# Kernel optimization log

Hardware: AMD Instinct MI355X
Metric: run time of the kernel (lower is better)

## Reference

```python
import jax, jax.numpy as jnp
import numpy as np

B, C, H, W, S = 32, 256, 80, 80, 2
MID = max(C // 4, 16)  # 64

def setup_inputs() -> dict:
    key = jax.random.key(0)
    k1, k2, k3, k4 = jax.random.split(key, 4)
    x = jax.random.normal(k1, (B, C, H, W), jnp.float32)
    w1 = jax.random.normal(k2, (MID, C), jnp.float32) * 0.05   # 1x1 conv, no bias
    w2 = jax.random.normal(k3, (2 * S * S, MID), jnp.float32) * 0.05
    b2 = jax.random.normal(k4, (2 * S * S,), jnp.float32) * 0.05
    return {"x": x, "w1": w1, "w2": w2, "b2": b2}

def _bilinear_border(im, gx, gy):
    # im: (C,H,W); gx,gy: (H,W) normalized coords in [-1,1]
    # matches F.grid_sample(mode='bilinear', padding_mode='border', align_corners=True)
    Hh, Ww = im.shape[1], im.shape[2]
    ix = jnp.clip((gx + 1.0) * 0.5 * (Ww - 1), 0.0, Ww - 1)  # border clamp
    iy = jnp.clip((gy + 1.0) * 0.5 * (Hh - 1), 0.0, Hh - 1)
    x0 = jnp.floor(ix); y0 = jnp.floor(iy)
    x0i = x0.astype(jnp.int32); y0i = y0.astype(jnp.int32)
    x1i = jnp.clip(x0i + 1, 0, Ww - 1); y1i = jnp.clip(y0i + 1, 0, Hh - 1)
    wx = ix - x0; wy = iy - y0
    v00 = im[:, y0i, x0i]; v01 = im[:, y0i, x1i]
    v10 = im[:, y1i, x0i]; v11 = im[:, y1i, x1i]
    return (v00 * (1 - wx) * (1 - wy) + v01 * wx * (1 - wy)
            + v10 * (1 - wx) * wy + v11 * wx * wy)

def _dysample(x, w1, w2, b2):
    Bb, Cc, Hh, Ww = x.shape
    s = S; ss = s * s
    # offset branch: 1x1 conv -> ReLU -> 1x1 conv -> tanh
    hid = jax.nn.relu(jnp.einsum('bchw,mc->bmhw', x, w1))
    off = jnp.tanh(jnp.einsum('bmhw,om->bohw', hid, w2) + b2[None, :, None, None])
    off_x, off_y = off[:, :ss], off[:, ss:]  # each (B,ss,H,W)
    H2, W2 = Hh * s, Ww * s
    ys = jnp.linspace(-1 + 1 / H2, 1 - 1 / H2, H2, dtype=x.dtype)
    xs = jnp.linspace(-1 + 1 / W2, 1 - 1 / W2, W2, dtype=x.dtype)
    gy, gx = jnp.meshgrid(ys, xs, indexing='ij')  # (H2,W2)
    def rearr(g):  # (H2,W2) -> (ss,H,W), matching the torch view/permute chain
        return g.reshape(Hh, s, Ww, s).transpose(0, 2, 1, 3).reshape(Hh, Ww, ss).transpose(2, 0, 1)
    gxb = rearr(gx)[None]; gyb = rearr(gy)[None]  # (1,ss,H,W)
    sf = 2.0 / max(H2, W2)
    sx = gxb + off_x * sf  # (B,ss,H,W)
    sy = gyb + off_y * sf
    # sample: each of the ss grids samples from the same image (no x replication)
    samp = jax.vmap(
        lambda im, gxs, gys: jax.vmap(lambda a, b: _bilinear_border(im, a, b))(gxs, gys)
    )(x, sx, sy)  # (B,ss,C,H,W)
    # pixel-shuffle rearrangement to (B,C,H*s,W*s)
    out = samp.transpose(0, 2, 1, 3, 4).reshape(Bb, Cc, s, s, Hh, Ww)
    out = out.transpose(0, 1, 4, 2, 5, 3).reshape(Bb, Cc, H2, W2)
    return out

def reference(x, w1, w2, b2):
    return _dysample(x, w1, w2, b2)
```

## Files before the change

### kernel.cpp

```cpp
#include <hip/hip_runtime.h>
#include <math.h>

#define B_   32
#define C_   256
#define H_   80
#define W_   80
#define MID_ 64
#define HW_  (H_*W_)
#define H2_  160
#define W2_  160
#define HW2_ (H2_*W2_)
#define CSPLIT_ 8
#define CCHUNK_ (C_/CSPLIT_)

__global__ __launch_bounds__(256) void transpose_w1_kernel(
    const float* __restrict__ w1, float* __restrict__ w1t)
{
    int idx = blockIdx.x * 256 + threadIdx.x;
    int m = idx & (MID_-1);
    int c = idx >> 6;
    w1t[idx] = w1[m*C_ + c];
}

__global__ __launch_bounds__(256) void offsets_kernel(
    const float* __restrict__ x, const float* __restrict__ w1t,
    const float* __restrict__ w2, const float* __restrict__ b2,
    float* __restrict__ off)
{
    int p  = blockIdx.x * 256 + threadIdx.x;
    int b  = p / HW_;
    int hw = p - b*HW_;
    const float* xp = x + (size_t)b*C_*HW_ + hw;

    float hid[MID_];
    #pragma unroll
    for (int m = 0; m < MID_; ++m) hid[m] = 0.f;

    for (int c = 0; c < C_; ++c) {
        float xv = xp[(size_t)c*HW_];
        const float* wr = w1t + c*MID_;
        #pragma unroll
        for (int m = 0; m < MID_; ++m) hid[m] = fmaf(xv, wr[m], hid[m]);
    }
    #pragma unroll
    for (int m = 0; m < MID_; ++m) hid[m] = fmaxf(hid[m], 0.f);

    float* op = off + (size_t)b*8*HW_ + hw;
    #pragma unroll
    for (int o = 0; o < 8; ++o) {
        float acc = b2[o];
        #pragma unroll
        for (int m = 0; m < MID_; ++m) acc = fmaf(hid[m], w2[o*MID_+m], acc);
        op[o*HW_] = tanhf(acc);
    }
}

__global__ __launch_bounds__(256) void sample_kernel(
    const float* __restrict__ x, const float* __restrict__ off,
    float* __restrict__ out)
{
    int p  = blockIdx.x * 256 + threadIdx.x;
    int b  = p / HW_;
    int hw = p - b*HW_;
    int h  = hw / W_;
    int w  = hw - h*W_;
    int c0 = blockIdx.y * CCHUNK_;

    const float* offp = off + (size_t)b*8*HW_ + hw;

    float wgt[4][4];
    int   ofs[4][4];
    #pragma unroll
    for (int k = 0; k < 4; ++k) {
        int i = k >> 1, j = k & 1;
        float ox = offp[k*HW_];
        float oy = offp[(4+k)*HW_];
        float gx = -1.f + (2.f*(float)(2*w+j) + 1.f) * (1.f/(float)W2_);
        float gy = -1.f + (2.f*(float)(2*h+i) + 1.f) * (1.f/(float)H2_);
        float sx = gx + ox * (2.f/(float)W2_);
        float sy = gy + oy * (2.f/(float)H2_);
        float ix = (sx + 1.f) * 0.5f * (float)(W_-1);
        float iy = (sy + 1.f) * 0.5f * (float)(H_-1);
        ix = fminf(fmaxf(ix, 0.f), (float)(W_-1));
        iy = fminf(fmaxf(iy, 0.f), (float)(H_-1));
        float xf = floorf(ix), yf = floorf(iy);
        int   x0 = (int)xf,    y0 = (int)yf;
        float wx = ix - xf,    wy = iy - yf;
        int   x1 = min(x0+1, W_-1), y1 = min(y0+1, H_-1);
        wgt[k][0] = (1.f-wx)*(1.f-wy);
        wgt[k][1] = wx*(1.f-wy);
        wgt[k][2] = (1.f-wx)*wy;
        wgt[k][3] = wx*wy;
        ofs[k][0] = y0*W_ + x0;
        ofs[k][1] = y0*W_ + x1;
        ofs[k][2] = y1*W_ + x0;
        ofs[k][3] = y1*W_ + x1;
    }

    const float* xq = x   + ((size_t)b*C_ + c0)*HW_;
    float*       oq = out + ((size_t)b*C_ + c0)*HW2_;
    int obase = (2*h)*W2_ + 2*w;

    #pragma unroll 2
    for (int ci = 0; ci < CCHUNK_; ++ci) {
        int xcb = ci*HW_;
        float v[4];
        #pragma unroll
        for (int k = 0; k < 4; ++k) {
            v[k] = xq[xcb + ofs[k][0]]*wgt[k][0] + xq[xcb + ofs[k][1]]*wgt[k][1]
                 + xq[xcb + ofs[k][2]]*wgt[k][2] + xq[xcb + ofs[k][3]]*wgt[k][3];
        }
        int ob = ci*HW2_ + obase;
        *reinterpret_cast<float2*>(oq + ob)        = make_float2(v[0], v[1]);
        *reinterpret_cast<float2*>(oq + ob + W2_)  = make_float2(v[2], v[3]);
    }
}

extern "C" void kernel_launch(void* const* d_in, const int* in_sizes, int n_in,
                              void* d_out, int out_size, void* d_ws, size_t ws_size,
                              hipStream_t stream) {
    const float* x  = (const float*)d_in[0];
    const float* w1 = (const float*)d_in[1];
    const float* w2 = (const float*)d_in[2];
    const float* b2 = (const float*)d_in[3];
    float* out = (float*)d_out;

    float* off = (float*)d_ws;
    float* w1t = off + (size_t)8*B_*HW_;

    const int npix = B_*HW_;

    transpose_w1_kernel<<<(C_*MID_)/256, 256, 0, stream>>>(w1, w1t);
    offsets_kernel<<<npix/256, 256, 0, stream>>>(x, w1t, w2, b2, off);
    dim3 grid2(npix/256, CSPLIT_);
    sample_kernel <<<grid2, 256, 0, stream>>>(x, off, out);
}
```

Baseline: 1.270 ms.

## Fuse offset computation and bilinear sampling with shared-memory row windows

Merges the offset MLP kernel and the sampling kernel into one kernel that keeps each pixel's offsets in registers. This drops the global offset buffer and the second launch. Each block handles a 4-row tile of one image and stages an 8-row window of input channels into LDS, 8 channels at a time, so the bilinear gathers read shared memory instead of global memory. In exchange, the grid shrinks to 640 blocks that each walk all channels serially, with a barrier every 8 channels, and the register pressure from the 64-wide hidden vector now sits alongside the sampling loop.

```diff
diff --git a/kernel.cpp b/kernel.cpp
--- a/kernel.cpp
+++ b/kernel.cpp
@@ -10,8 +10,12 @@
 #define H2_  160
 #define W2_  160
 #define HW2_ (H2_*W2_)
-#define CSPLIT_ 8
-#define CCHUNK_ (C_/CSPLIT_)
+
+#define TILE_H 4
+#define WIN_H  8
+#define WINSZ  (WIN_H*W_)
+#define NCH    8
+#define TPB    (TILE_H*W_)
 
 __global__ __launch_bounds__(256) void transpose_w1_kernel(
     const float* __restrict__ w1, float* __restrict__ w1t)
@@ -22,22 +26,36 @@
     w1t[idx] = w1[m*C_ + c];
 }
 
-__global__ __launch_bounds__(256) void offsets_kernel(
+__global__ __launch_bounds__(TPB) void fused_kernel(
     const float* __restrict__ x, const float* __restrict__ w1t,
     const float* __restrict__ w2, const float* __restrict__ b2,
-    float* __restrict__ off)
+    float* __restrict__ out)
 {
-    int p  = blockIdx.x * 256 + threadIdx.x;
-    int b  = p / HW_;
-    int hw = p - b*HW_;
+    __shared__ float xs[NCH * WINSZ];
+
+    const int blk = blockIdx.x;
+    const int b   = blk / (H_/TILE_H);
+    const int t   = blk % (H_/TILE_H);
+    const int h0  = t * TILE_H;
+    const int ty  = threadIdx.x / W_;
+    const int tx  = threadIdx.x - ty*W_;
+    const int h   = h0 + ty;
+    const int w   = tx;
+    const int hw  = h*W_ + w;
+
+    int y_lo = (79*h0)/80 - 1;
+    if (y_lo < 0) y_lo = 0;
+    if (y_lo > H_ - WIN_H) y_lo = H_ - WIN_H;
+
     const float* xp = x + (size_t)b*C_*HW_ + hw;
 
     float hid[MID_];
     #pragma unroll
     for (int m = 0; m < MID_; ++m) hid[m] = 0.f;
 
+    #pragma unroll 4
     for (int c = 0; c < C_; ++c) {
-        float xv = xp[(size_t)c*HW_];
+        float xv = xp[c*HW_];
         const float* wr = w1t + c*MID_;
         #pragma unroll
         for (int m = 0; m < MID_; ++m) hid[m] = fmaf(xv, wr[m], hid[m]);
@@ -45,40 +63,24 @@
     #pragma unroll
     for (int m = 0; m < MID_; ++m) hid[m] = fmaxf(hid[m], 0.f);
 
-    float* op = off + (size_t)b*8*HW_ + hw;
+    float offv[8];
     #pragma unroll
     for (int o = 0; o < 8; ++o) {
         float acc = b2[o];
         #pragma unroll
         for (int m = 0; m < MID_; ++m) acc = fmaf(hid[m], w2[o*MID_+m], acc);
-        op[o*HW_] = tanhf(acc);
+        offv[o] = tanhf(acc);
     }
-}
 
-__global__ __launch_bounds__(256) void sample_kernel(
-    const float* __restrict__ x, const float* __restrict__ off,
-    float* __restrict__ out)
-{
-    int p  = blockIdx.x * 256 + threadIdx.x;
-    int b  = p / HW_;
-    int hw = p - b*HW_;
-    int h  = hw / W_;
-    int w  = hw - h*W_;
-    int c0 = blockIdx.y * CCHUNK_;
-
-    const float* offp = off + (size_t)b*8*HW_ + hw;
-
-    float wgt[4][4];
-    int   ofs[4][4];
+    float wgt[16];
+    int   idx[16];
     #pragma unroll
     for (int k = 0; k < 4; ++k) {
         int i = k >> 1, j = k & 1;
-        float ox = offp[k*HW_];
-        float oy = offp[(4+k)*HW_];
         float gx = -1.f + (2.f*(float)(2*w+j) + 1.f) * (1.f/(float)W2_);
         float gy = -1.f + (2.f*(float)(2*h+i) + 1.f) * (1.f/(float)H2_);
-        float sx = gx + ox * (2.f/(float)W2_);
-        float sy = gy + oy * (2.f/(float)H2_);
+        float sx = gx + offv[k]   * (2.f/(float)W2_);
+        float sy = gy + offv[4+k] * (2.f/(float)H2_);
         float ix = (sx + 1.f) * 0.5f * (float)(W_-1);
         float iy = (sy + 1.f) * 0.5f * (float)(H_-1);
         ix = fminf(fmaxf(ix, 0.f), (float)(W_-1));
@@ -87,32 +89,45 @@
         int   x0 = (int)xf,    y0 = (int)yf;
         float wx = ix - xf,    wy = iy - yf;
         int   x1 = min(x0+1, W_-1), y1 = min(y0+1, H_-1);
-        wgt[k][0] = (1.f-wx)*(1.f-wy);
-        wgt[k][1] = wx*(1.f-wy);
-        wgt[k][2] = (1.f-wx)*wy;
-        wgt[k][3] = wx*wy;
-        ofs[k][0] = y0*W_ + x0;
-        ofs[k][1] = y0*W_ + x1;
-        ofs[k][2] = y1*W_ + x0;
-        ofs[k][3] = y1*W_ + x1;
+        int   ly0 = y0 - y_lo,      ly1 = y1 - y_lo;
+        wgt[k*4+0] = (1.f-wx)*(1.f-wy);
+        wgt[k*4+1] = wx*(1.f-wy);
+        wgt[k*4+2] = (1.f-wx)*wy;
+        wgt[k*4+3] = wx*wy;
+        idx[k*4+0] = ly0*W_ + x0;
+        idx[k*4+1] = ly0*W_ + x1;
+        idx[k*4+2] = ly1*W_ + x0;
+        idx[k*4+3] = ly1*W_ + x1;
     }
 
-    const float* xq = x   + ((size_t)b*C_ + c0)*HW_;
-    float*       oq = out + ((size_t)b*C_ + c0)*HW2_;
-    int obase = (2*h)*W2_ + 2*w;
+    const float* xgb = x + (size_t)b*C_*HW_ + y_lo*W_;
+    const int ob_off = (2*h)*W2_ + 2*w;
 
-    #pragma unroll 2
-    for (int ci = 0; ci < CCHUNK_; ++ci) {
-        int xcb = ci*HW_;
-        float v[4];
+    for (int c0 = 0; c0 < C_; c0 += NCH) {
+        __syncthreads();
         #pragma unroll
-        for (int k = 0; k < 4; ++k) {
-            v[k] = xq[xcb + ofs[k][0]]*wgt[k][0] + xq[xcb + ofs[k][1]]*wgt[k][1]
-                 + xq[xcb + ofs[k][2]]*wgt[k][2] + xq[xcb + ofs[k][3]]*wgt[k][3];
+        for (int ch = 0; ch < NCH; ++ch) {
+            float2 s = *reinterpret_cast<const float2*>(
+                xgb + (size_t)(c0+ch)*HW_ + 2*threadIdx.x);
+            *reinterpret_cast<float2*>(&xs[ch*WINSZ + 2*threadIdx.x]) = s;
         }
-        int ob = ci*HW2_ + obase;
-        *reinterpret_cast<float2*>(oq + ob)        = make_float2(v[0], v[1]);
-        *reinterpret_cast<float2*>(oq + ob + W2_)  = make_float2(v[2], v[3]);
+        __syncthreads();
+
+        #pragma unroll
+        for (int ch = 0; ch < NCH; ++ch) {
+            const float* cs = &xs[ch*WINSZ];
+            float v0 = cs[idx[0]] *wgt[0]  + cs[idx[1]] *wgt[1]
+                     + cs[idx[2]] *wgt[2]  + cs[idx[3]] *wgt[3];
+            float v1 = cs[idx[4]] *wgt[4]  + cs[idx[5]] *wgt[5]
+                     + cs[idx[6]] *wgt[6]  + cs[idx[7]] *wgt[7];
+            float v2 = cs[idx[8]] *wgt[8]  + cs[idx[9]] *wgt[9]
+                     + cs[idx[10]]*wgt[10] + cs[idx[11]]*wgt[11];
+            float v3 = cs[idx[12]]*wgt[12] + cs[idx[13]]*wgt[13]
+                     + cs[idx[14]]*wgt[14] + cs[idx[15]]*wgt[15];
+            float* ob = out + (size_t)(b*C_ + c0 + ch)*HW2_ + ob_off;
+            *reinterpret_cast<float2*>(ob)       = make_float2(v0, v1);
+            *reinterpret_cast<float2*>(ob + W2_) = make_float2(v2, v3);
+        }
     }
 }
 
@@ -124,14 +139,10 @@
     const float* w2 = (const float*)d_in[2];
     const float* b2 = (const float*)d_in[3];
     float* out = (float*)d_out;
-
-    float* off = (float*)d_ws;
-    float* w1t = off + (size_t)8*B_*HW_;
-
-    const int npix = B_*HW_;
+    float* w1t = (float*)d_ws;
 
     transpose_w1_kernel<<<(C_*MID_)/256, 256, 0, stream>>>(w1, w1t);
-    offsets_kernel<<<npix/256, 256, 0, stream>>>(x, w1t, w2, b2, off);
-    dim3 grid2(npix/256, CSPLIT_);
-    sample_kernel <<<grid2, 256, 0, stream>>>(x, off, out);
+
+    const int nblk = B_ * (H_/TILE_H);
+    fused_kernel<<<nblk, TPB, 0, stream>>>(x, w1t, w2, b2, out);
 }
```

Result: faster. 1.103 ms (-13.1%).
